# Kernel tuning notes

Hardware: AMD Instinct MI355X
Metric: run time of the kernel (lower is better)

Reference implementation:

```python
import jax, jax.numpy as jnp
import numpy as np

B, S, D, H = 2, 2048, 1024, 16
DK = D // H


def setup_inputs() -> dict:
    key = jax.random.key(0)
    ks = jax.random.split(key, 11)
    std = 1.0 / np.sqrt(D)
    inp = {
        "q": jax.random.normal(ks[0], (B, S, D), jnp.float32),
        "k": jax.random.normal(ks[1], (B, S, D), jnp.float32),
        "v": jax.random.normal(ks[2], (B, S, D), jnp.float32),
        # causal mask, broadcast over batch and heads; masked_fill where mask==0
        "mask": jnp.tril(jnp.ones((S, S), dtype=bool))[None, None, :, :],
        "Wq": jax.random.uniform(ks[3], (D, D), jnp.float32, -std, std),
        "bq": jax.random.uniform(ks[4], (D,), jnp.float32, -std, std),
        "Wk": jax.random.uniform(ks[5], (D, D), jnp.float32, -std, std),
        "bk": jax.random.uniform(ks[6], (D,), jnp.float32, -std, std),
        "Wv": jax.random.uniform(ks[7], (D, D), jnp.float32, -std, std),
        "bv": jax.random.uniform(ks[8], (D,), jnp.float32, -std, std),
        "Wo": jax.random.uniform(ks[9], (D, D), jnp.float32, -std, std),
        "bo": jax.random.uniform(ks[10], (D,), jnp.float32, -std, std),
    }
    return inp


def reference(q, k, v, mask, Wq, bq, Wk, bk, Wv, bv, Wo, bo):
    b, s, _ = q.shape
    # projections, split heads: [B,S,D] -> [B,H,S,dk]
    def proj(x, W, bias):
        return (x @ W + bias).reshape(b, -1, H, DK).transpose(0, 2, 1, 3)
    qh, kh, vh = proj(q, Wq, bq), proj(k, Wk, bk), proj(v, Wv, bv)
    scale = 1.0 / np.sqrt(DK)
    scores = jnp.einsum("bhqd,bhkd->bhqk", qh, kh) * scale  # [B,H,S,S]
    scores = jnp.where(mask, scores, jnp.float32(-1e9))
    attn = jax.nn.softmax(scores, axis=-1)
    out = jnp.einsum("bhqk,bhkd->bhqd", attn, vh)  # [B,H,S,dk]
    concat = out.transpose(0, 2, 1, 3).reshape(b, s, D)
    return concat @ Wo + bo
```

## Files before the change

### kernel.cpp

```cpp
#include <hip/hip_runtime.h>


typedef short v8s  __attribute__((ext_vector_type(8)));
typedef short v4ss __attribute__((ext_vector_type(4)));
typedef float v4f  __attribute__((ext_vector_type(4)));
typedef unsigned int v2u __attribute__((ext_vector_type(2)));

#define S_LEN 2048
#define D_DIM 1024
#define NHEAD 16
#define DK 64
#define M_ROWS 4096

__device__ inline unsigned short f2bf(float f) {
    unsigned x;
    __builtin_memcpy(&x, &f, 4);
    unsigned r = x + 0x7fffu + ((x >> 16) & 1u);
    return (unsigned short)(r >> 16);
}

__device__ inline unsigned cvtpk_bf16(float lo, float hi) {
    unsigned d;
    asm("v_cvt_pk_bf16_f32 %0, %1, %2" : "=v"(d) : "v"(lo), "v"(hi));
    return d;
}

__device__ inline void gload_lds16(const void* g, void* l) {
    __builtin_amdgcn_global_load_lds(
        (const __attribute__((address_space(1))) unsigned int*)g,
        (__attribute__((address_space(3))) unsigned int*)l, 16, 0, 0);
}

__global__ __launch_bounds__(256) void prep(
    const float* __restrict__ q, const float* __restrict__ k,
    const float* __restrict__ v,
    const float* __restrict__ W0, const float* __restrict__ W1,
    const float* __restrict__ W2, const float* __restrict__ W3,
    unsigned short* __restrict__ Xb, unsigned short* __restrict__ Wt)
{
    __shared__ unsigned short t[64][72];
    const int id = blockIdx.x;

    if (id < 6144) {
        const int z = id >> 11;
        const int x = id & 2047;
        const float* X = (z == 0) ? q : (z == 1) ? k : v;
        const size_t off = ((size_t)x * 256 + threadIdx.x) * 8;
        float4 f0 = *(const float4*)(X + off);
        float4 f1 = *(const float4*)(X + off + 4);
        v8s p;
        p[0]=(short)f2bf(f0.x); p[1]=(short)f2bf(f0.y); p[2]=(short)f2bf(f0.z); p[3]=(short)f2bf(f0.w);
        p[4]=(short)f2bf(f1.x); p[5]=(short)f2bf(f1.y); p[6]=(short)f2bf(f1.z); p[7]=(short)f2bf(f1.w);
        *(v8s*)(Xb + (size_t)z * M_ROWS * D_DIM + off) = p;
        return;
    }

    const int tt = id - 6144;
    const int z  = tt >> 8;
    const int rem = tt & 255;
    const int bx = rem & 15;
    const int by = rem >> 4;
    const float* W = (z == 0) ? W0 : (z == 1) ? W1 : (z == 2) ? W2 : W3;
    unsigned short* dst = Wt + (size_t)z * D_DIM * D_DIM;

    const int n0 = bx * 64, k0 = by * 64;
    const int tid = threadIdx.x;
    const int lr = tid >> 4;
    const int lc = (tid & 15) * 4;

#pragma unroll
    for (int kk = 0; kk < 64; kk += 16) {
        float4 f = *(const float4*)(W + (size_t)(k0 + kk + lr) * D_DIM + n0 + lc);
        t[lc + 0][kk + lr] = f2bf(f.x);
        t[lc + 1][kk + lr] = f2bf(f.y);
        t[lc + 2][kk + lr] = f2bf(f.z);
        t[lc + 3][kk + lr] = f2bf(f.w);
    }
    __syncthreads();
    const int wr = tid >> 2;
    const int wc = (tid & 3) * 16;
    v8s o0, o1;
#pragma unroll
    for (int e = 0; e < 8; e++) { o0[e] = t[wr][wc + e]; o1[e] = t[wr][wc + 8 + e]; }
    *(v8s*)(dst + (size_t)(n0 + wr) * D_DIM + k0 + wc)     = o0;
    *(v8s*)(dst + (size_t)(n0 + wr) * D_DIM + k0 + wc + 8) = o1;
}

__global__ __launch_bounds__(256) void gemm_qkv(
    const unsigned short* __restrict__ Xb,
    const unsigned short* __restrict__ Wt,
    const float* __restrict__ bq, const float* __restrict__ bk,
    const float* __restrict__ bv,
    unsigned short* __restrict__ Qp, unsigned short* __restrict__ Kp,
    unsigned short* __restrict__ Vt)
{
    const int id   = blockIdx.x;
    const int xcd  = id & 7;
    const int slot = id >> 3;
    const int nblk = slot & 7;
    const int mg   = (slot >> 3) & 3;
    const int z    = slot >> 5;
    const int mblk = mg * 8 + xcd;

    const unsigned short* X = Xb + (size_t)z * M_ROWS * D_DIM;
    const unsigned short* W = Wt + (size_t)z * D_DIM * D_DIM;
    const float* bias = (z == 0) ? bq : (z == 1) ? bk : bv;

    __shared__ unsigned short lds_a[3][128 * 32];
    __shared__ unsigned short lds_b[3][128 * 32];

    const int tid  = threadIdx.x;
    const int lane = tid & 63;
    const int wave = tid >> 6;
    const int wm   = wave >> 1;
    const int wn   = wave & 1;
    const int quad = lane >> 4;
    const int col  = lane & 15;
    const int m0   = mblk * 128;
    const int n0   = nblk * 128;

    v4f acc[4][4];
#pragma unroll
    for (int i = 0; i < 4; i++)
#pragma unroll
        for (int j = 0; j < 4; j++)
#pragma unroll
            for (int r = 0; r < 4; r++) acc[i][j][r] = 0.0f;

    const int srow = wave * 16 + (lane >> 2);
    const int schk = (lane & 3) * 8;
    const int soff = wave * 512 + lane * 8;

    const unsigned short* Xr0 = X + (size_t)(m0 + srow) * D_DIM + schk;
    const unsigned short* Xr1 = X + (size_t)(m0 + 64 + srow) * D_DIM + schk;
    const unsigned short* Wr0 = W + (size_t)(n0 + srow) * D_DIM + schk;
    const unsigned short* Wr1 = W + (size_t)(n0 + 64 + srow) * D_DIM + schk;

    auto stage = [&](unsigned short* A, unsigned short* B, int k0) {
        gload_lds16(Xr0 + k0, A + soff);
        gload_lds16(Xr1 + k0, A + soff + 2048);
        gload_lds16(Wr0 + k0, B + soff);
        gload_lds16(Wr1 + k0, B + soff + 2048);
    };

    auto compute = [&](const unsigned short* A, const unsigned short* B) {
        v8s af[4], bf[4];
#pragma unroll
        for (int mt = 0; mt < 4; mt++)
            af[mt] = *(const v8s*)(A + (wm * 64 + mt * 16 + col) * 32 + quad * 8);
#pragma unroll
        for (int nt = 0; nt < 4; nt++)
            bf[nt] = *(const v8s*)(B + (wn * 64 + nt * 16 + col) * 32 + quad * 8);
#pragma unroll
        for (int mt = 0; mt < 4; mt++)
#pragma unroll
            for (int nt = 0; nt < 4; nt++)
                acc[mt][nt] = __builtin_amdgcn_mfma_f32_16x16x32_bf16(
                    af[mt], bf[nt], acc[mt][nt], 0, 0, 0);
    };

    stage(lds_a[0], lds_b[0], 0);
    stage(lds_a[1], lds_b[1], 32);

    unsigned short *ra = lds_a[0], *rb = lds_b[0];
    unsigned short *pa = lds_a[1], *pb = lds_b[1];
    unsigned short *sa = lds_a[2], *sb = lds_b[2];

    for (int k0 = 0; k0 < 992; k0 += 32) {
        asm volatile("s_waitcnt vmcnt(4)" ::: "memory");
        asm volatile("s_waitcnt lgkmcnt(0)" ::: "memory");
        __builtin_amdgcn_sched_barrier(0);
        __builtin_amdgcn_s_barrier();
        __builtin_amdgcn_sched_barrier(0);
        if (k0 + 64 < 1024) stage(sa, sb, k0 + 64);
        compute(ra, rb);
        unsigned short* t;
        t = ra; ra = pa; pa = sa; sa = t;
        t = rb; rb = pb; pb = sb; sb = t;
    }
    asm volatile("s_waitcnt vmcnt(0)" ::: "memory");
    asm volatile("s_waitcnt lgkmcnt(0)" ::: "memory");
    __builtin_amdgcn_sched_barrier(0);
    __builtin_amdgcn_s_barrier();
    __builtin_amdgcn_sched_barrier(0);
    compute(ra, rb);

    int   nn[4];
    float bvv[4];
#pragma unroll
    for (int nt = 0; nt < 4; nt++) {
        nn[nt]  = n0 + wn * 64 + nt * 16 + col;
        bvv[nt] = bias[nn[nt]];
    }

    if (z < 2) {
        unsigned short* out = (z == 0) ? Qp : Kp;
#pragma unroll
        for (int mt = 0; mt < 4; mt++) {
#pragma unroll
            for (int nt = 0; nt < 4; nt++) {
                const int h  = nn[nt] >> 6;
                const int dk = nn[nt] & 63;
#pragma unroll
                for (int r = 0; r < 4; r++) {
                    int row = m0 + wm * 64 + mt * 16 + quad * 4 + r;
                    int b   = row >> 11, t = row & 2047;
                    out[(((size_t)(b * NHEAD + h) * S_LEN) + t) * DK + dk] =
                        f2bf(acc[mt][nt][r] + bvv[nt]);
                }
            }
        }
    } else {
#pragma unroll
        for (int mt = 0; mt < 4; mt++) {
#pragma unroll
            for (int nt = 0; nt < 4; nt++) {
                const int h  = nn[nt] >> 6;
                const int dk = nn[nt] & 63;
                int row = m0 + wm * 64 + mt * 16 + quad * 4;
                int b   = row >> 11, t = row & 2047;
                v4ss pk;
#pragma unroll
                for (int r = 0; r < 4; r++) pk[r] = (short)f2bf(acc[mt][nt][r] + bvv[nt]);
                *(v4ss*)(Vt + ((size_t)(b * NHEAD + h) * DK + dk) * S_LEN + t) = pk;
            }
        }
    }
}

__global__ __launch_bounds__(128) void flash10(
    const unsigned short* __restrict__ Qp,
    const unsigned short* __restrict__ Kp,
    const unsigned short* __restrict__ Vt,
    unsigned short* __restrict__ Op)
{
    __shared__ __align__(16) unsigned char smem[9216];

    const int tid  = threadIdx.x;
    const int wave = tid >> 6;
    const int lane = tid & 63;
    const int quad = lane >> 4;
    const int col  = lane & 15;

    unsigned short* pw = (unsigned short*)smem + wave * (32 * 72);

    const int i   = blockIdx.x;
    const int xcd = i & 7;
    const int j   = i >> 3;
    const int bh  = xcd * 4 + (j & 3);
    const int q32 = 63 - (j >> 2);
    const int r0  = q32 * 32;

    const unsigned short* Qh = Qp + (size_t)bh * S_LEN * DK;
    const unsigned short* Kh = Kp + (size_t)bh * S_LEN * DK;
    const unsigned short* Vh = Vt + (size_t)bh * DK * S_LEN;

    v8s qf[2][2];
#pragma unroll
    for (int mt = 0; mt < 2; mt++)
#pragma unroll
        for (int c = 0; c < 2; c++)
            qf[mt][c] = *(const v8s*)(Qh + (size_t)(r0 + mt * 16 + col) * DK + c * 32 + quad * 8);

    float lpart[2] = {0.f, 0.f};
    v4f acc_o[2][4];
#pragma unroll
    for (int mt = 0; mt < 2; mt++)
#pragma unroll
        for (int nt = 0; nt < 4; nt++)
#pragma unroll
            for (int r = 0; r < 4; r++) acc_o[mt][nt][r] = 0.0f;

    const float CS = 0.18033688f;
    const float CM = 28.8539008f;

    const int nsteps = (q32 >> 1) + 1;

    v8s kc[2][4];
    const int kvp = wave * 64;
#pragma unroll
    for (int c = 0; c < 2; c++)
#pragma unroll
        for (int nt = 0; nt < 4; nt++)
            kc[c][nt] = *(const v8s*)(Kh + (size_t)(kvp + nt * 16 + col) * DK + c * 32 + quad * 8);

    for (int step = wave; step < nsteps; step += 2) {
        const int kv0 = step * 64;
        const int kvn = (step + 2 < nsteps) ? kv0 + 128 : kv0;

        v8s vf[2][4];
#pragma unroll
        for (int c = 0; c < 2; c++)
#pragma unroll
            for (int nt = 0; nt < 4; nt++)
                vf[c][nt] = *(const v8s*)(Vh + (size_t)(nt * 16 + col) * S_LEN + kv0 + c * 32 + quad * 8);
        v8s kn[2][4];
#pragma unroll
        for (int c = 0; c < 2; c++)
#pragma unroll
            for (int nt = 0; nt < 4; nt++)
                kn[c][nt] = *(const v8s*)(Kh + (size_t)(kvn + nt * 16 + col) * DK + c * 32 + quad * 8);

#pragma unroll
        for (int mt = 0; mt < 2; mt++) {
            v4f s[4];
            __builtin_amdgcn_s_setprio(1);
#pragma unroll
            for (int nt = 0; nt < 4; nt++) {
#pragma unroll
                for (int r = 0; r < 4; r++) s[nt][r] = 0.0f;
#pragma unroll
                for (int c = 0; c < 2; c++)
                    s[nt] = __builtin_amdgcn_mfma_f32_16x16x32_bf16(kc[c][nt], qf[mt][c], s[nt], 0, 0, 0);
            }
            __builtin_amdgcn_s_setprio(0);

            const int rbase = r0 + mt * 16;
            float lp = 0.f;
            if (kv0 + 64 > rbase) {
#pragma unroll
                for (int nt = 0; nt < 4; nt++) {
#pragma unroll
                    for (int r = 0; r < 4; r++) {
                        float p = __builtin_amdgcn_exp2f(fmaf(s[nt][r], CS, -CM));
                        if (kv0 + nt * 16 + quad * 4 + r > rbase + col) p = 0.0f;
                        s[nt][r] = p;
                        lp += p;
                    }
                }
            } else {
#pragma unroll
                for (int nt = 0; nt < 4; nt++) {
#pragma unroll
                    for (int r = 0; r < 4; r++) {
                        float p = __builtin_amdgcn_exp2f(fmaf(s[nt][r], CS, -CM));
                        s[nt][r] = p;
                        lp += p;
                    }
                }
            }
            lpart[mt] += lp;

#pragma unroll
            for (int nt = 0; nt < 4; nt++) {
                unsigned u0 = cvtpk_bf16(s[nt][0], s[nt][1]);
                unsigned u1 = cvtpk_bf16(s[nt][2], s[nt][3]);
                v2u w; w[0] = u0; w[1] = u1;
                *(v2u*)(pw + (mt * 16 + col) * 72 + nt * 16 + quad * 4) = w;
            }
        }

        __builtin_amdgcn_s_setprio(1);
#pragma unroll
        for (int mt = 0; mt < 2; mt++) {
#pragma unroll
            for (int c = 0; c < 2; c++) {
                v8s af = *(const v8s*)(pw + (mt * 16 + col) * 72 + c * 32 + quad * 8);
#pragma unroll
                for (int nt = 0; nt < 4; nt++)
                    acc_o[mt][nt] = __builtin_amdgcn_mfma_f32_16x16x32_bf16(af, vf[c][nt], acc_o[mt][nt], 0, 0, 0);
            }
        }
        __builtin_amdgcn_s_setprio(0);

#pragma unroll
        for (int c = 0; c < 2; c++)
#pragma unroll
            for (int nt = 0; nt < 4; nt++)
                kc[c][nt] = kn[c][nt];
    }

#pragma unroll
    for (int mt = 0; mt < 2; mt++) {
        lpart[mt] += __shfl_xor(lpart[mt], 16);
        lpart[mt] += __shfl_xor(lpart[mt], 32);
    }

    float* comb = (float*)smem;
    __syncthreads();
    if (wave == 1) {
        float* dst = comb + lane * 34;
#pragma unroll
        for (int mt = 0; mt < 2; mt++)
#pragma unroll
            for (int nt = 0; nt < 4; nt++)
                *(v4f*)(dst + (mt * 4 + nt) * 4) = acc_o[mt][nt];
        dst[32] = lpart[0];
        dst[33] = lpart[1];
    }
    __syncthreads();
    if (wave != 0) return;

    {
        const float* src = comb + lane * 34;
#pragma unroll
        for (int mt = 0; mt < 2; mt++)
#pragma unroll
            for (int nt = 0; nt < 4; nt++) {
                v4f o = *(const v4f*)(src + (mt * 4 + nt) * 4);
#pragma unroll
                for (int r = 0; r < 4; r++) acc_o[mt][nt][r] += o[r];
            }
        lpart[0] += src[32];
        lpart[1] += src[33];
    }

    lpart[0] = 1.0f / lpart[0];
    lpart[1] = 1.0f / lpart[1];
    float li[2][4];
#pragma unroll
    for (int mt = 0; mt < 2; mt++)
#pragma unroll
        for (int r = 0; r < 4; r++)
            li[mt][r] = __shfl(lpart[mt], quad * 4 + r);

#pragma unroll
    for (int mt = 0; mt < 2; mt++) {
#pragma unroll
        for (int nt = 0; nt < 4; nt++) {
#pragma unroll
            for (int r = 0; r < 4; r++) {
                size_t addr = ((size_t)bh * S_LEN + r0 + mt * 16 + quad * 4 + r) * DK + nt * 16 + col;
                Op[addr] = f2bf(acc_o[mt][nt][r] * li[mt][r]);
            }
        }
    }
}

__global__ __launch_bounds__(256) void gemm_out(
    const unsigned short* __restrict__ Ap,
    const unsigned short* __restrict__ Wot,
    const float* __restrict__ bo,
    float* __restrict__ out)
{
    __shared__ unsigned short lds_a[3][64 * 32];
    __shared__ unsigned short lds_b[3][128 * 32];

    const int id   = blockIdx.x;
    const int xcd  = id & 7;
    const int slot = id >> 3;
    const int nblk = slot & 7;
    const int mg   = slot >> 3;
    const int mblk = mg * 8 + xcd;

    const int tid  = threadIdx.x;
    const int lane = tid & 63;
    const int wave = tid >> 6;
    const int wm   = wave >> 1;
    const int wn   = wave & 1;
    const int quad = lane >> 4;
    const int col  = lane & 15;
    const int m0   = mblk * 64;
    const int n0   = nblk * 128;

    v4f acc[2][4];
#pragma unroll
    for (int i = 0; i < 2; i++)
#pragma unroll
        for (int j = 0; j < 4; j++)
#pragma unroll
            for (int r = 0; r < 4; r++) acc[i][j][r] = 0.0f;

    const int srow = wave * 16 + (lane >> 2);
    const int schk = (lane & 3) * 8;
    const int soff = wave * 512 + lane * 8;

    const int tokA = m0 + srow;
    const int bbA  = tokA >> 11, ttA = tokA & 2047;
    const unsigned short* Abase = Ap + ((size_t)bbA * NHEAD * S_LEN + ttA) * DK;
    const unsigned short* Wr0 = Wot + (size_t)(n0 + srow) * D_DIM + schk;
    const unsigned short* Wr1 = Wot + (size_t)(n0 + 64 + srow) * D_DIM + schk;

    auto stage = [&](unsigned short* A, unsigned short* B, int k0) {
        const int h_  = k0 >> 6;
        const int dk_ = (k0 & 63) + schk;
        gload_lds16(Abase + (size_t)h_ * S_LEN * DK + dk_, A + soff);
        gload_lds16(Wr0 + k0, B + soff);
        gload_lds16(Wr1 + k0, B + soff + 2048);
    };

    auto compute = [&](const unsigned short* A, const unsigned short* B) {
        v8s af[2], bf[4];
#pragma unroll
        for (int mt = 0; mt < 2; mt++)
            af[mt] = *(const v8s*)(A + (wm * 32 + mt * 16 + col) * 32 + quad * 8);
#pragma unroll
        for (int nt = 0; nt < 4; nt++)
            bf[nt] = *(const v8s*)(B + (wn * 64 + nt * 16 + col) * 32 + quad * 8);
#pragma unroll
        for (int mt = 0; mt < 2; mt++)
#pragma unroll
            for (int nt = 0; nt < 4; nt++)
                acc[mt][nt] = __builtin_amdgcn_mfma_f32_16x16x32_bf16(
                    af[mt], bf[nt], acc[mt][nt], 0, 0, 0);
    };

    stage(lds_a[0], lds_b[0], 0);
    stage(lds_a[1], lds_b[1], 32);

    unsigned short *ra = lds_a[0], *rb = lds_b[0];
    unsigned short *pa = lds_a[1], *pb = lds_b[1];
    unsigned short *sa = lds_a[2], *sb = lds_b[2];

    for (int k0 = 0; k0 < 992; k0 += 32) {
        asm volatile("s_waitcnt vmcnt(3)" ::: "memory");
        asm volatile("s_waitcnt lgkmcnt(0)" ::: "memory");
        __builtin_amdgcn_sched_barrier(0);
        __builtin_amdgcn_s_barrier();
        __builtin_amdgcn_sched_barrier(0);
        if (k0 + 64 < 1024) stage(sa, sb, k0 + 64);
        compute(ra, rb);
        unsigned short* t;
        t = ra; ra = pa; pa = sa; sa = t;
        t = rb; rb = pb; pb = sb; sb = t;
    }
    asm volatile("s_waitcnt vmcnt(0)" ::: "memory");
    asm volatile("s_waitcnt lgkmcnt(0)" ::: "memory");
    __builtin_amdgcn_sched_barrier(0);
    __builtin_amdgcn_s_barrier();
    __builtin_amdgcn_sched_barrier(0);
    compute(ra, rb);

    float bvv[4];
    int   nn[4];
#pragma unroll
    for (int nt = 0; nt < 4; nt++) {
        nn[nt]  = n0 + wn * 64 + nt * 16 + col;
        bvv[nt] = bo[nn[nt]];
    }

#pragma unroll
    for (int mt = 0; mt < 2; mt++) {
#pragma unroll
        for (int nt = 0; nt < 4; nt++) {
#pragma unroll
            for (int r = 0; r < 4; r++) {
                int row = m0 + wm * 32 + mt * 16 + quad * 4 + r;
                out[(size_t)row * D_DIM + nn[nt]] = acc[mt][nt][r] + bvv[nt];
            }
        }
    }
}

extern "C" void kernel_launch(void* const* d_in, const int* in_sizes, int n_in,
                              void* d_out, int out_size, void* d_ws, size_t ws_size,
                              hipStream_t stream) {
    const float* q  = (const float*)d_in[0];
    const float* k  = (const float*)d_in[1];
    const float* v  = (const float*)d_in[2];
    const float* Wq = (const float*)d_in[4];
    const float* bq = (const float*)d_in[5];
    const float* Wk = (const float*)d_in[6];
    const float* bk = (const float*)d_in[7];
    const float* Wv = (const float*)d_in[8];
    const float* bv = (const float*)d_in[9];
    const float* Wo = (const float*)d_in[10];
    const float* bo = (const float*)d_in[11];
    float* out = (float*)d_out;

    unsigned short* ws = (unsigned short*)d_ws;
    const size_t WT   = (size_t)D_DIM * D_DIM;
    const size_t TENS = (size_t)M_ROWS * D_DIM;
    unsigned short* Wt = ws;
    unsigned short* Qp = ws + 4 * WT;
    unsigned short* Kp = Qp + TENS;
    unsigned short* Vt = Kp + TENS;
    unsigned short* Xb = Vt + TENS;
    unsigned short* Ap = Xb;

    prep<<<7168, 256, 0, stream>>>(q, k, v, Wq, Wk, Wv, Wo, Xb, Wt);
    gemm_qkv<<<768, 256, 0, stream>>>(Xb, Wt, bq, bk, bv, Qp, Kp, Vt);
    flash10<<<2048, 128, 0, stream>>>(Qp, Kp, Vt, Ap);
    gemm_out<<<512, 256, 0, stream>>>(Ap, Wt + 3 * WT, bo, out);
}
```

Before: 255.6 us.

## Pair heavy and light causal query tiles per block and split KV across four waves

```diff
diff --git a/kernel.cpp b/kernel.cpp
--- a/kernel.cpp
+++ b/kernel.cpp
@@ -228,13 +228,13 @@
     }
 }
 
-__global__ __launch_bounds__(128) void flash10(
+__global__ __launch_bounds__(256) void flash11(
     const unsigned short* __restrict__ Qp,
     const unsigned short* __restrict__ Kp,
     const unsigned short* __restrict__ Vt,
     unsigned short* __restrict__ Op)
 {
-    __shared__ __align__(16) unsigned char smem[9216];
+    __shared__ __align__(16) unsigned char smem[18432];
 
     const int tid  = threadIdx.x;
     const int wave = tid >> 6;
@@ -248,183 +248,196 @@
     const int xcd = i & 7;
     const int j   = i >> 3;
     const int bh  = xcd * 4 + (j & 3);
-    const int q32 = 63 - (j >> 2);
-    const int r0  = q32 * 32;
+    const int pr  = j >> 2;
 
     const unsigned short* Qh = Qp + (size_t)bh * S_LEN * DK;
     const unsigned short* Kh = Kp + (size_t)bh * S_LEN * DK;
     const unsigned short* Vh = Vt + (size_t)bh * DK * S_LEN;
 
-    v8s qf[2][2];
-#pragma unroll
-    for (int mt = 0; mt < 2; mt++)
-#pragma unroll
-        for (int c = 0; c < 2; c++)
-            qf[mt][c] = *(const v8s*)(Qh + (size_t)(r0 + mt * 16 + col) * DK + c * 32 + quad * 8);
-
-    float lpart[2] = {0.f, 0.f};
-    v4f acc_o[2][4];
-#pragma unroll
-    for (int mt = 0; mt < 2; mt++)
-#pragma unroll
-        for (int nt = 0; nt < 4; nt++)
-#pragma unroll
-            for (int r = 0; r < 4; r++) acc_o[mt][nt][r] = 0.0f;
-
     const float CS = 0.18033688f;
     const float CM = 28.8539008f;
 
-    const int nsteps = (q32 >> 1) + 1;
-
-    v8s kc[2][4];
-    const int kvp = wave * 64;
-#pragma unroll
-    for (int c = 0; c < 2; c++)
-#pragma unroll
-        for (int nt = 0; nt < 4; nt++)
-            kc[c][nt] = *(const v8s*)(Kh + (size_t)(kvp + nt * 16 + col) * DK + c * 32 + quad * 8);
-
-    for (int step = wave; step < nsteps; step += 2) {
-        const int kv0 = step * 64;
-        const int kvn = (step + 2 < nsteps) ? kv0 + 128 : kv0;
-
-        v8s vf[2][4];
+    float* cb0 = (float*)smem;
+    float* cb1 = cb0 + 64 * 34;
+
+    auto process = [&](int q32) {
+        const int r0 = q32 * 32;
+        const int nsteps = (q32 >> 1) + 1;
+
+        v8s qf[2][2];
+#pragma unroll
+        for (int mt = 0; mt < 2; mt++)
+#pragma unroll
+            for (int c = 0; c < 2; c++)
+                qf[mt][c] = *(const v8s*)(Qh + (size_t)(r0 + mt * 16 + col) * DK + c * 32 + quad * 8);
+
+        float lpart[2] = {0.f, 0.f};
+        v4f acc_o[2][4];
+#pragma unroll
+        for (int mt = 0; mt < 2; mt++)
+#pragma unroll
+            for (int nt = 0; nt < 4; nt++)
+#pragma unroll
+                for (int r = 0; r < 4; r++) acc_o[mt][nt][r] = 0.0f;
+
+        v8s kc[2][4];
+        const int kvp = wave * 64;
 #pragma unroll
         for (int c = 0; c < 2; c++)
 #pragma unroll
             for (int nt = 0; nt < 4; nt++)
-                vf[c][nt] = *(const v8s*)(Vh + (size_t)(nt * 16 + col) * S_LEN + kv0 + c * 32 + quad * 8);
-        v8s kn[2][4];
-#pragma unroll
-        for (int c = 0; c < 2; c++)
-#pragma unroll
-            for (int nt = 0; nt < 4; nt++)
-                kn[c][nt] = *(const v8s*)(Kh + (size_t)(kvn + nt * 16 + col) * DK + c * 32 + quad * 8);
+                kc[c][nt] = *(const v8s*)(Kh + (size_t)(kvp + nt * 16 + col) * DK + c * 32 + quad * 8);
+
+        for (int step = wave; step < nsteps; step += 4) {
+            const int kv0 = step * 64;
+            const int kvn = (step + 4 < nsteps) ? kv0 + 256 : kv0;
+
+            v8s vf[2][4];
+#pragma unroll
+            for (int c = 0; c < 2; c++)
+#pragma unroll
+                for (int nt = 0; nt < 4; nt++)
+                    vf[c][nt] = *(const v8s*)(Vh + (size_t)(nt * 16 + col) * S_LEN + kv0 + c * 32 + quad * 8);
+            v8s kn[2][4];
+#pragma unroll
+            for (int c = 0; c < 2; c++)
+#pragma unroll
+                for (int nt = 0; nt < 4; nt++)
+                    kn[c][nt] = *(const v8s*)(Kh + (size_t)(kvn + nt * 16 + col) * DK + c * 32 + quad * 8);
+
+#pragma unroll
+            for (int mt = 0; mt < 2; mt++) {
+                v4f s[4];
+                __builtin_amdgcn_s_setprio(1);
+#pragma unroll
+                for (int nt = 0; nt < 4; nt++) {
+#pragma unroll
+                    for (int r = 0; r < 4; r++) s[nt][r] = 0.0f;
+#pragma unroll
+                    for (int c = 0; c < 2; c++)
+                        s[nt] = __builtin_amdgcn_mfma_f32_16x16x32_bf16(kc[c][nt], qf[mt][c], s[nt], 0, 0, 0);
+                }
+                __builtin_amdgcn_s_setprio(0);
+
+                const int rbase = r0 + mt * 16;
+                float lp = 0.f;
+                if (kv0 + 64 > rbase) {
+#pragma unroll
+                    for (int nt = 0; nt < 4; nt++) {
+#pragma unroll
+                        for (int r = 0; r < 4; r++) {
+                            float p = __builtin_amdgcn_exp2f(fmaf(s[nt][r], CS, -CM));
+                            if (kv0 + nt * 16 + quad * 4 + r > rbase + col) p = 0.0f;
+                            s[nt][r] = p;
+                            lp += p;
+                        }
+                    }
+                } else {
+#pragma unroll
+                    for (int nt = 0; nt < 4; nt++) {
+#pragma unroll
+                        for (int r = 0; r < 4; r++) {
+                            float p = __builtin_amdgcn_exp2f(fmaf(s[nt][r], CS, -CM));
+                            s[nt][r] = p;
+                            lp += p;
+                        }
+                    }
+                }
+                lpart[mt] += lp;
+
+#pragma unroll
+                for (int nt = 0; nt < 4; nt++) {
+                    unsigned u0 = cvtpk_bf16(s[nt][0], s[nt][1]);
+                    unsigned u1 = cvtpk_bf16(s[nt][2], s[nt][3]);
+                    v2u w; w[0] = u0; w[1] = u1;
+                    *(v2u*)(pw + (mt * 16 + col) * 72 + nt * 16 + quad * 4) = w;
+                }
+            }
+
+            __builtin_amdgcn_s_setprio(1);
+#pragma unroll
+            for (int mt = 0; mt < 2; mt++) {
+#pragma unroll
+                for (int c = 0; c < 2; c++) {
+                    v8s af = *(const v8s*)(pw + (mt * 16 + col) * 72 + c * 32 + quad * 8);
+#pragma unroll
+                    for (int nt = 0; nt < 4; nt++)
+                        acc_o[mt][nt] = __builtin_amdgcn_mfma_f32_16x16x32_bf16(af, vf[c][nt], acc_o[mt][nt], 0, 0, 0);
+                }
+            }
+            __builtin_amdgcn_s_setprio(0);
+
+#pragma unroll
+            for (int c = 0; c < 2; c++)
+#pragma unroll
+                for (int nt = 0; nt < 4; nt++)
+                    kc[c][nt] = kn[c][nt];
+        }
 
 #pragma unroll
         for (int mt = 0; mt < 2; mt++) {
-            v4f s[4];
-            __builtin_amdgcn_s_setprio(1);
-#pragma unroll
-            for (int nt = 0; nt < 4; nt++) {
-#pragma unroll
-                for (int r = 0; r < 4; r++) s[nt][r] = 0.0f;
-#pragma unroll
-                for (int c = 0; c < 2; c++)
-                    s[nt] = __builtin_amdgcn_mfma_f32_16x16x32_bf16(kc[c][nt], qf[mt][c], s[nt], 0, 0, 0);
-            }
-            __builtin_amdgcn_s_setprio(0);
-
-            const int rbase = r0 + mt * 16;
-            float lp = 0.f;
-            if (kv0 + 64 > rbase) {
+            lpart[mt] += __shfl_xor(lpart[mt], 16);
+            lpart[mt] += __shfl_xor(lpart[mt], 32);
+        }
+
+        auto store_part = [&](float* dst) {
+#pragma unroll
+            for (int mt = 0; mt < 2; mt++)
+#pragma unroll
+                for (int nt = 0; nt < 4; nt++)
+                    *(v4f*)(dst + (mt * 4 + nt) * 4) = acc_o[mt][nt];
+            dst[32] = lpart[0];
+            dst[33] = lpart[1];
+        };
+        auto add_part = [&](const float* src) {
+#pragma unroll
+            for (int mt = 0; mt < 2; mt++)
 #pragma unroll
                 for (int nt = 0; nt < 4; nt++) {
+                    v4f o = *(const v4f*)(src + (mt * 4 + nt) * 4);
+#pragma unroll
+                    for (int r = 0; r < 4; r++) acc_o[mt][nt][r] += o[r];
+                }
+            lpart[0] += src[32];
+            lpart[1] += src[33];
+        };
+
+        __syncthreads();
+        if (wave == 1)      store_part(cb0 + lane * 34);
+        else if (wave == 3) store_part(cb1 + lane * 34);
+        __syncthreads();
+        if (wave == 0)      add_part(cb0 + lane * 34);
+        else if (wave == 2) add_part(cb1 + lane * 34);
+        __syncthreads();
+        if (wave == 2)      store_part(cb0 + lane * 34);
+        __syncthreads();
+        if (wave == 0) {
+            add_part(cb0 + lane * 34);
+            float i0 = 1.0f / lpart[0];
+            float i1 = 1.0f / lpart[1];
+            float li[2][4];
+#pragma unroll
+            for (int r = 0; r < 4; r++) {
+                li[0][r] = __shfl(i0, quad * 4 + r);
+                li[1][r] = __shfl(i1, quad * 4 + r);
+            }
+#pragma unroll
+            for (int mt = 0; mt < 2; mt++) {
+#pragma unroll
+                for (int nt = 0; nt < 4; nt++) {
 #pragma unroll
                     for (int r = 0; r < 4; r++) {
-                        float p = __builtin_amdgcn_exp2f(fmaf(s[nt][r], CS, -CM));
-                        if (kv0 + nt * 16 + quad * 4 + r > rbase + col) p = 0.0f;
-                        s[nt][r] = p;
-                        lp += p;
+                        size_t addr = ((size_t)bh * S_LEN + r0 + mt * 16 + quad * 4 + r) * DK + nt * 16 + col;
+                        Op[addr] = f2bf(acc_o[mt][nt][r] * li[mt][r]);
                     }
                 }
-            } else {
-#pragma unroll
-                for (int nt = 0; nt < 4; nt++) {
-#pragma unroll
-                    for (int r = 0; r < 4; r++) {
-                        float p = __builtin_amdgcn_exp2f(fmaf(s[nt][r], CS, -CM));
-                        s[nt][r] = p;
-                        lp += p;
-                    }
-                }
-            }
-            lpart[mt] += lp;
-
-#pragma unroll
-            for (int nt = 0; nt < 4; nt++) {
-                unsigned u0 = cvtpk_bf16(s[nt][0], s[nt][1]);
-                unsigned u1 = cvtpk_bf16(s[nt][2], s[nt][3]);
-                v2u w; w[0] = u0; w[1] = u1;
-                *(v2u*)(pw + (mt * 16 + col) * 72 + nt * 16 + quad * 4) = w;
             }
         }
-
-        __builtin_amdgcn_s_setprio(1);
-#pragma unroll
-        for (int mt = 0; mt < 2; mt++) {
-#pragma unroll
-            for (int c = 0; c < 2; c++) {
-                v8s af = *(const v8s*)(pw + (mt * 16 + col) * 72 + c * 32 + quad * 8);
-#pragma unroll
-                for (int nt = 0; nt < 4; nt++)
-                    acc_o[mt][nt] = __builtin_amdgcn_mfma_f32_16x16x32_bf16(af, vf[c][nt], acc_o[mt][nt], 0, 0, 0);
-            }
-        }
-        __builtin_amdgcn_s_setprio(0);
-
-#pragma unroll
-        for (int c = 0; c < 2; c++)
-#pragma unroll
-            for (int nt = 0; nt < 4; nt++)
-                kc[c][nt] = kn[c][nt];
-    }
-
-#pragma unroll
-    for (int mt = 0; mt < 2; mt++) {
-        lpart[mt] += __shfl_xor(lpart[mt], 16);
-        lpart[mt] += __shfl_xor(lpart[mt], 32);
-    }
-
-    float* comb = (float*)smem;
-    __syncthreads();
-    if (wave == 1) {
-        float* dst = comb + lane * 34;
-#pragma unroll
-        for (int mt = 0; mt < 2; mt++)
-#pragma unroll
-            for (int nt = 0; nt < 4; nt++)
-                *(v4f*)(dst + (mt * 4 + nt) * 4) = acc_o[mt][nt];
-        dst[32] = lpart[0];
-        dst[33] = lpart[1];
-    }
-    __syncthreads();
-    if (wave != 0) return;
-
-    {
-        const float* src = comb + lane * 34;
-#pragma unroll
-        for (int mt = 0; mt < 2; mt++)
-#pragma unroll
-            for (int nt = 0; nt < 4; nt++) {
-                v4f o = *(const v4f*)(src + (mt * 4 + nt) * 4);
-#pragma unroll
-                for (int r = 0; r < 4; r++) acc_o[mt][nt][r] += o[r];
-            }
-        lpart[0] += src[32];
-        lpart[1] += src[33];
-    }
-
-    lpart[0] = 1.0f / lpart[0];
-    lpart[1] = 1.0f / lpart[1];
-    float li[2][4];
-#pragma unroll
-    for (int mt = 0; mt < 2; mt++)
-#pragma unroll
-        for (int r = 0; r < 4; r++)
-            li[mt][r] = __shfl(lpart[mt], quad * 4 + r);
-
-#pragma unroll
-    for (int mt = 0; mt < 2; mt++) {
-#pragma unroll
-        for (int nt = 0; nt < 4; nt++) {
-#pragma unroll
-            for (int r = 0; r < 4; r++) {
-                size_t addr = ((size_t)bh * S_LEN + r0 + mt * 16 + quad * 4 + r) * DK + nt * 16 + col;
-                Op[addr] = f2bf(acc_o[mt][nt][r] * li[mt][r]);
-            }
-        }
-    }
+        __syncthreads();
+    };
+
+    process(63 - pr);
+    process(pr);
 }
 
 __global__ __launch_bounds__(256) void gemm_out(
@@ -570,6 +583,6 @@
 
     prep<<<7168, 256, 0, stream>>>(q, k, v, Wq, Wk, Wv, Wo, Xb, Wt);
     gemm_qkv<<<768, 256, 0, stream>>>(Xb, Wt, bq, bk, bv, Qp, Kp, Vt);
-    flash10<<<2048, 128, 0, stream>>>(Qp, Kp, Vt, Ap);
+    flash11<<<1024, 256, 0, stream>>>(Qp, Kp, Vt, Ap);
     gemm_out<<<512, 256, 0, stream>>>(Ap, Wt + 3 * WT, bo, out);
 }
```

After: 262.7 us. 2.8% more time.

## Pair causal query tiles per block to balance work and share K/V loads

Applied to the files above, without the earlier changes.

```diff
diff --git a/kernel.cpp b/kernel.cpp
--- a/kernel.cpp
+++ b/kernel.cpp
@@ -228,13 +228,13 @@
     }
 }
 
-__global__ __launch_bounds__(128) void flash10(
+__global__ __launch_bounds__(128) void flash12(
     const unsigned short* __restrict__ Qp,
     const unsigned short* __restrict__ Kp,
     const unsigned short* __restrict__ Vt,
     unsigned short* __restrict__ Op)
 {
-    __shared__ __align__(16) unsigned char smem[9216];
+    __shared__ __align__(16) unsigned char smem[18432];
 
     const int tid  = threadIdx.x;
     const int wave = tid >> 6;
@@ -242,40 +242,44 @@
     const int quad = lane >> 4;
     const int col  = lane & 15;
 
-    unsigned short* pw = (unsigned short*)smem + wave * (32 * 72);
+    unsigned short* pwA = (unsigned short*)smem + wave * 2 * (32 * 72);
+    unsigned short* pwB = pwA + 32 * 72;
 
     const int i   = blockIdx.x;
     const int xcd = i & 7;
     const int j   = i >> 3;
     const int bh  = xcd * 4 + (j & 3);
-    const int q32 = 63 - (j >> 2);
-    const int r0  = q32 * 32;
+    const int pr  = j >> 2;
+    const int q32a = 63 - pr, q32b = pr;
+    const int r0a = q32a * 32, r0b = q32b * 32;
+    const int nsA = (q32a >> 1) + 1;
+    const int nsB = (q32b >> 1) + 1;
 
     const unsigned short* Qh = Qp + (size_t)bh * S_LEN * DK;
     const unsigned short* Kh = Kp + (size_t)bh * S_LEN * DK;
     const unsigned short* Vh = Vt + (size_t)bh * DK * S_LEN;
 
-    v8s qf[2][2];
+    v8s qfa[2][2], qfb[2][2];
 #pragma unroll
     for (int mt = 0; mt < 2; mt++)
 #pragma unroll
-        for (int c = 0; c < 2; c++)
-            qf[mt][c] = *(const v8s*)(Qh + (size_t)(r0 + mt * 16 + col) * DK + c * 32 + quad * 8);
-
-    float lpart[2] = {0.f, 0.f};
-    v4f acc_o[2][4];
+        for (int c = 0; c < 2; c++) {
+            qfa[mt][c] = *(const v8s*)(Qh + (size_t)(r0a + mt * 16 + col) * DK + c * 32 + quad * 8);
+            qfb[mt][c] = *(const v8s*)(Qh + (size_t)(r0b + mt * 16 + col) * DK + c * 32 + quad * 8);
+        }
+
+    float lpa[2] = {0.f, 0.f}, lpb[2] = {0.f, 0.f};
+    v4f acca[2][4], accb[2][4];
 #pragma unroll
     for (int mt = 0; mt < 2; mt++)
 #pragma unroll
         for (int nt = 0; nt < 4; nt++)
 #pragma unroll
-            for (int r = 0; r < 4; r++) acc_o[mt][nt][r] = 0.0f;
+            for (int r = 0; r < 4; r++) { acca[mt][nt][r] = 0.0f; accb[mt][nt][r] = 0.0f; }
 
     const float CS = 0.18033688f;
     const float CM = 28.8539008f;
 
-    const int nsteps = (q32 >> 1) + 1;
-
     v8s kc[2][4];
     const int kvp = wave * 64;
 #pragma unroll
@@ -284,9 +288,10 @@
         for (int nt = 0; nt < 4; nt++)
             kc[c][nt] = *(const v8s*)(Kh + (size_t)(kvp + nt * 16 + col) * DK + c * 32 + quad * 8);
 
-    for (int step = wave; step < nsteps; step += 2) {
+    for (int step = wave; step < nsA; step += 2) {
         const int kv0 = step * 64;
-        const int kvn = (step + 2 < nsteps) ? kv0 + 128 : kv0;
+        const int kvn = (step + 2 < nsA) ? kv0 + 128 : kv0;
+        const bool doB = (step < nsB);
 
         v8s vf[2][4];
 #pragma unroll
@@ -311,15 +316,15 @@
                 for (int r = 0; r < 4; r++) s[nt][r] = 0.0f;
 #pragma unroll
                 for (int c = 0; c < 2; c++)
-                    s[nt] = __builtin_amdgcn_mfma_f32_16x16x32_bf16(kc[c][nt], qf[mt][c], s[nt], 0, 0, 0);
+                    s[nt] = __builtin_amdgcn_mfma_f32_16x16x32_bf16(kc[c][nt], qfa[mt][c], s[nt], 0, 0, 0);
             }
             __builtin_amdgcn_s_setprio(0);
 
-            const int rbase = r0 + mt * 16;
+            const int rbase = r0a + mt * 16;
             float lp = 0.f;
             if (kv0 + 64 > rbase) {
 #pragma unroll
-                for (int nt = 0; nt < 4; nt++) {
+                for (int nt = 0; nt < 4; nt++)
 #pragma unroll
                     for (int r = 0; r < 4; r++) {
                         float p = __builtin_amdgcn_exp2f(fmaf(s[nt][r], CS, -CM));
@@ -327,39 +332,96 @@
                         s[nt][r] = p;
                         lp += p;
                     }
-                }
             } else {
 #pragma unroll
-                for (int nt = 0; nt < 4; nt++) {
+                for (int nt = 0; nt < 4; nt++)
 #pragma unroll
                     for (int r = 0; r < 4; r++) {
                         float p = __builtin_amdgcn_exp2f(fmaf(s[nt][r], CS, -CM));
                         s[nt][r] = p;
                         lp += p;
                     }
-                }
-            }
-            lpart[mt] += lp;
+            }
+            lpa[mt] += lp;
 
 #pragma unroll
             for (int nt = 0; nt < 4; nt++) {
                 unsigned u0 = cvtpk_bf16(s[nt][0], s[nt][1]);
                 unsigned u1 = cvtpk_bf16(s[nt][2], s[nt][3]);
                 v2u w; w[0] = u0; w[1] = u1;
-                *(v2u*)(pw + (mt * 16 + col) * 72 + nt * 16 + quad * 4) = w;
+                *(v2u*)(pwA + (mt * 16 + col) * 72 + nt * 16 + quad * 4) = w;
+            }
+        }
+
+        if (doB) {
+#pragma unroll
+            for (int mt = 0; mt < 2; mt++) {
+                v4f s[4];
+                __builtin_amdgcn_s_setprio(1);
+#pragma unroll
+                for (int nt = 0; nt < 4; nt++) {
+#pragma unroll
+                    for (int r = 0; r < 4; r++) s[nt][r] = 0.0f;
+#pragma unroll
+                    for (int c = 0; c < 2; c++)
+                        s[nt] = __builtin_amdgcn_mfma_f32_16x16x32_bf16(kc[c][nt], qfb[mt][c], s[nt], 0, 0, 0);
+                }
+                __builtin_amdgcn_s_setprio(0);
+
+                const int rbase = r0b + mt * 16;
+                float lp = 0.f;
+                if (kv0 + 64 > rbase) {
+#pragma unroll
+                    for (int nt = 0; nt < 4; nt++)
+#pragma unroll
+                        for (int r = 0; r < 4; r++) {
+                            float p = __builtin_amdgcn_exp2f(fmaf(s[nt][r], CS, -CM));
+                            if (kv0 + nt * 16 + quad * 4 + r > rbase + col) p = 0.0f;
+                            s[nt][r] = p;
+                            lp += p;
+                        }
+                } else {
+#pragma unroll
+                    for (int nt = 0; nt < 4; nt++)
+#pragma unroll
+                        for (int r = 0; r < 4; r++) {
+                            float p = __builtin_amdgcn_exp2f(fmaf(s[nt][r], CS, -CM));
+                            s[nt][r] = p;
+                            lp += p;
+                        }
+                }
+                lpb[mt] += lp;
+
+#pragma unroll
+                for (int nt = 0; nt < 4; nt++) {
+                    unsigned u0 = cvtpk_bf16(s[nt][0], s[nt][1]);
+                    unsigned u1 = cvtpk_bf16(s[nt][2], s[nt][3]);
+                    v2u w; w[0] = u0; w[1] = u1;
+                    *(v2u*)(pwB + (mt * 16 + col) * 72 + nt * 16 + quad * 4) = w;
+                }
             }
         }
 
         __builtin_amdgcn_s_setprio(1);
 #pragma unroll
-        for (int mt = 0; mt < 2; mt++) {
+        for (int mt = 0; mt < 2; mt++)
 #pragma unroll
             for (int c = 0; c < 2; c++) {
-                v8s af = *(const v8s*)(pw + (mt * 16 + col) * 72 + c * 32 + quad * 8);
+                v8s af = *(const v8s*)(pwA + (mt * 16 + col) * 72 + c * 32 + quad * 8);
 #pragma unroll
                 for (int nt = 0; nt < 4; nt++)
-                    acc_o[mt][nt] = __builtin_amdgcn_mfma_f32_16x16x32_bf16(af, vf[c][nt], acc_o[mt][nt], 0, 0, 0);
-            }
+                    acca[mt][nt] = __builtin_amdgcn_mfma_f32_16x16x32_bf16(af, vf[c][nt], acca[mt][nt], 0, 0, 0);
+            }
+        if (doB) {
+#pragma unroll
+            for (int mt = 0; mt < 2; mt++)
+#pragma unroll
+                for (int c = 0; c < 2; c++) {
+                    v8s af = *(const v8s*)(pwB + (mt * 16 + col) * 72 + c * 32 + quad * 8);
+#pragma unroll
+                    for (int nt = 0; nt < 4; nt++)
+                        accb[mt][nt] = __builtin_amdgcn_mfma_f32_16x16x32_bf16(af, vf[c][nt], accb[mt][nt], 0, 0, 0);
+                }
         }
         __builtin_amdgcn_s_setprio(0);
 
@@ -372,47 +434,54 @@
 
 #pragma unroll
     for (int mt = 0; mt < 2; mt++) {
-        lpart[mt] += __shfl_xor(lpart[mt], 16);
-        lpart[mt] += __shfl_xor(lpart[mt], 32);
+        lpa[mt] += __shfl_xor(lpa[mt], 16);
+        lpa[mt] += __shfl_xor(lpa[mt], 32);
+        lpb[mt] += __shfl_xor(lpb[mt], 16);
+        lpb[mt] += __shfl_xor(lpb[mt], 32);
     }
 
     float* comb = (float*)smem;
     __syncthreads();
     if (wave == 1) {
-        float* dst = comb + lane * 34;
+        float* dst = comb + lane * 68;
 #pragma unroll
         for (int mt = 0; mt < 2; mt++)
 #pragma unroll
-            for (int nt = 0; nt < 4; nt++)
-                *(v4f*)(dst + (mt * 4 + nt) * 4) = acc_o[mt][nt];
-        dst[32] = lpart[0];
-        dst[33] = lpart[1];
+            for (int nt = 0; nt < 4; nt++) {
+                *(v4f*)(dst + (mt * 4 + nt) * 4)      = acca[mt][nt];
+                *(v4f*)(dst + 34 + (mt * 4 + nt) * 4) = accb[mt][nt];
+            }
+        dst[32] = lpa[0]; dst[33] = lpa[1];
+        dst[66] = lpb[0]; dst[67] = lpb[1];
     }
     __syncthreads();
     if (wave != 0) return;
 
     {
-        const float* src = comb + lane * 34;
+        const float* src = comb + lane * 68;
 #pragma unroll
         for (int mt = 0; mt < 2; mt++)
 #pragma unroll
             for (int nt = 0; nt < 4; nt++) {
-                v4f o = *(const v4f*)(src + (mt * 4 + nt) * 4);
-#pragma unroll
-                for (int r = 0; r < 4; r++) acc_o[mt][nt][r] += o[r];
-            }
-        lpart[0] += src[32];
-        lpart[1] += src[33];
-    }
-
-    lpart[0] = 1.0f / lpart[0];
-    lpart[1] = 1.0f / lpart[1];
-    float li[2][4];
+                v4f oa = *(const v4f*)(src + (mt * 4 + nt) * 4);
+                v4f ob = *(const v4f*)(src + 34 + (mt * 4 + nt) * 4);
+#pragma unroll
+                for (int r = 0; r < 4; r++) { acca[mt][nt][r] += oa[r]; accb[mt][nt][r] += ob[r]; }
+            }
+        lpa[0] += src[32]; lpa[1] += src[33];
+        lpb[0] += src[66]; lpb[1] += src[67];
+    }
+
+    lpa[0] = 1.0f / lpa[0];  lpa[1] = 1.0f / lpa[1];
+    lpb[0] = 1.0f / lpb[0];  lpb[1] = 1.0f / lpb[1];
+    float lia[2][4], lib[2][4];
 #pragma unroll
     for (int mt = 0; mt < 2; mt++)
 #pragma unroll
-        for (int r = 0; r < 4; r++)
-            li[mt][r] = __shfl(lpart[mt], quad * 4 + r);
+        for (int r = 0; r < 4; r++) {
+            lia[mt][r] = __shfl(lpa[mt], quad * 4 + r);
+            lib[mt][r] = __shfl(lpb[mt], quad * 4 + r);
+        }
 
 #pragma unroll
     for (int mt = 0; mt < 2; mt++) {
@@ -420,8 +489,10 @@
         for (int nt = 0; nt < 4; nt++) {
 #pragma unroll
             for (int r = 0; r < 4; r++) {
-                size_t addr = ((size_t)bh * S_LEN + r0 + mt * 16 + quad * 4 + r) * DK + nt * 16 + col;
-                Op[addr] = f2bf(acc_o[mt][nt][r] * li[mt][r]);
+                size_t aA = ((size_t)bh * S_LEN + r0a + mt * 16 + quad * 4 + r) * DK + nt * 16 + col;
+                Op[aA] = f2bf(acca[mt][nt][r] * lia[mt][r]);
+                size_t aB = ((size_t)bh * S_LEN + r0b + mt * 16 + quad * 4 + r) * DK + nt * 16 + col;
+                Op[aB] = f2bf(accb[mt][nt][r] * lib[mt][r]);
             }
         }
     }
@@ -570,6 +641,6 @@
 
     prep<<<7168, 256, 0, stream>>>(q, k, v, Wq, Wk, Wv, Wo, Xb, Wt);
     gemm_qkv<<<768, 256, 0, stream>>>(Xb, Wt, bq, bk, bv, Qp, Kp, Vt);
-    flash10<<<2048, 128, 0, stream>>>(Qp, Kp, Vt, Ap);
+    flash12<<<1024, 128, 0, stream>>>(Qp, Kp, Vt, Ap);
     gemm_out<<<512, 256, 0, stream>>>(Ap, Wt + 3 * WT, bo, out);
 }
```

Measured after the change: 237.1 us. -7.2%, faster.
